# Performance work log

Hardware: AMD Instinct MI355X
Metric: run time of the kernel (lower is better)

Reference implementation:

```python
import jax, jax.numpy as jnp
import numpy as np

HIDDEN_DIM = 128
NEIGHBOR_K = 2
N_ROWS = 1_000_000
BATCH = 262_144


def setup_inputs() -> dict:
    key = jax.random.key(0)
    k1, k2, k3, k4 = jax.random.split(key, 4)
    D = HIDDEN_DIM
    cat = D * (2 * NEIGHBOR_K + 1)  # 640
    x_rows = jax.random.normal(k1, (N_ROWS, D), dtype=jnp.float32)
    seed_indices = jax.random.randint(k2, (BATCH,), 0, N_ROWS)
    # torch.nn.Linear params: W [out, in], b [out]
    W1 = jax.random.normal(k3, (D, cat), dtype=jnp.float32) * (1.0 / np.sqrt(cat))
    b1 = jnp.zeros((D,), dtype=jnp.float32)
    W2 = jax.random.normal(k4, (D, D), dtype=jnp.float32) * (1.0 / np.sqrt(D))
    b2 = jnp.zeros((D,), dtype=jnp.float32)
    return {"x_rows": x_rows, "seed_indices": seed_indices,
            "W1": W1, "b1": b1, "W2": W2, "b2": b2}


def reference(x_rows, seed_indices, W1, b1, W2, b2):
    N, D = x_rows.shape
    B = seed_indices.shape[0]
    offsets = jnp.arange(-NEIGHBOR_K, NEIGHBOR_K + 1)  # [2k+1]
    idx = jnp.clip(seed_indices[:, None] + offsets[None, :], 0, N - 1)  # [B, 2k+1]
    # gather neighbor rows and flatten -> same as torch.cat(chunks, dim=-1)
    x_cat = x_rows[idx].reshape(B, (2 * NEIGHBOR_K + 1) * D)  # [B, 5D]
    h = jax.nn.relu(x_cat @ W1.T + b1)  # [B, D]
    return h @ W2.T + b2  # [B, D]
```

## Files before the change

### kernel.cpp

```cpp
#include <hip/hip_runtime.h>
#include <hip/hip_bf16.h>

#define D 128
#define CAT 640
#define BM 32
#define W1F_ELEMS 81920
#define W2F_ELEMS 16384

typedef __attribute__((ext_vector_type(8))) short bf16x8;
typedef __attribute__((ext_vector_type(4))) float f32x4;

static __device__ __forceinline__ unsigned short f32_to_bf16(float f) {
    unsigned u = __float_as_uint(f);
    unsigned r = u + 0x7FFFu + ((u >> 16) & 1u);
    return (unsigned short)(r >> 16);
}

static __device__ __forceinline__ unsigned pack_bf16x2(float a, float b) {
    __hip_bfloat162 h = __float22bfloat162_rn(make_float2(a, b));
    return *reinterpret_cast<unsigned*>(&h);
}

static __device__ __forceinline__ void gload_lds16(const float* g, void* lds) {
    __builtin_amdgcn_global_load_lds(
        (const __attribute__((address_space(1))) void*)g,
        (__attribute__((address_space(3))) void*)lds, 16, 0, 0);
}

__global__ void prep_frags(const float* __restrict__ W1, const float* __restrict__ W2,
                           unsigned short* __restrict__ W1f, unsigned short* __restrict__ W2f) {
    int f = blockIdx.x * 256 + threadIdx.x;
    if (f < W1F_ELEMS) {
        int e = f & 7, l = (f >> 3) & 63, j16 = (f >> 9) & 7, ks = f >> 12;
        int o = j16 * 16 + (l & 15);
        int k = ks * 32 + ((l >> 4) << 3) + e;
        W1f[f] = f32_to_bf16(W1[o * CAT + k]);
    } else if (f < W1F_ELEMS + W2F_ELEMS) {
        int f2 = f - W1F_ELEMS;
        int e = f2 & 7, l = (f2 >> 3) & 63, j16 = (f2 >> 9) & 7, ks = f2 >> 12;
        int o = j16 * 16 + (l & 15);
        int k = ks * 32 + ((l >> 4) << 3) + e;
        W2f[f2] = f32_to_bf16(W2[o * D + k]);
    }
}

__global__ __launch_bounds__(256, 4) void rowmlp_kernel(
    const float* __restrict__ x_rows, const int* __restrict__ seeds,
    const unsigned short* __restrict__ W1f, const float* __restrict__ b1,
    const unsigned short* __restrict__ W2f, const float* __restrict__ b2,
    float* __restrict__ out, int Nrows)
{
    __shared__ __align__(16) unsigned char Ab[2][16384];
    __shared__ __align__(16) unsigned short Hb[16][D];
    __shared__ int sseed[BM];

    const int tid = threadIdx.x;
    const int blk = blockIdx.x;
    const int w   = tid >> 6;
    const int l   = tid & 63;
    const int l15 = l & 15;
    const int lhi = l >> 4;

    if (tid < BM) sseed[tid] = seeds[blk * BM + tid];
    __syncthreads();

    const int sb  = sseed[((w >> 1) << 4) + l15];
    const int ksb = (w & 1) * 2;

    const bf16x8* W1v = (const bf16x8*)W1f;
    const bf16x8* W2v = (const bf16x8*)W2f;

#define WAIT0 asm volatile("s_waitcnt vmcnt(0)" ::: "memory")
#define BAR   __builtin_amdgcn_s_barrier()

#define ISSUE(J, BUF)                                                          \
    {                                                                          \
        int idx = sb + (J) - 2;                                                \
        idx = idx < 0 ? 0 : (idx >= Nrows ? Nrows - 1 : idx);                  \
        const float* rp = x_rows + (size_t)idx * D + lhi * 8;                  \
        unsigned char* dst = Ab[BUF] + w * 4096;                               \
        gload_lds16(rp + (ksb + 0) * 32 + 0, dst + 0 * 1024);                  \
        gload_lds16(rp + (ksb + 0) * 32 + 4, dst + 1 * 1024);                  \
        gload_lds16(rp + (ksb + 1) * 32 + 0, dst + 2 * 1024);                  \
        gload_lds16(rp + (ksb + 1) * 32 + 4, dst + 3 * 1024);                  \
    }

#define LOADW1(J, RB)                                                          \
    {                                                                          \
        _Pragma("unroll")                                                      \
        for (int ks = 0; ks < 4; ++ks)                                         \
            _Pragma("unroll")                                                  \
            for (int n = 0; n < 2; ++n)                                        \
                w1r[RB][ks][n] = W1v[(((J) * 4 + ks) * 8 + (w * 2 + n)) * 64 + l]; \
    }

#define COMPUTE(BUF, RB)                                                       \
    {                                                                          \
        const float* fb = (const float*)Ab[BUF];                               \
        _Pragma("unroll")                                                      \
        for (int ks = 0; ks < 4; ++ks) {                                       \
            bf16x8 a[2];                                                       \
            _Pragma("unroll")                                                  \
            for (int m = 0; m < 2; ++m) {                                      \
                float4 q0 = *(const float4*)(fb + (m * 8 + ks * 2 + 0) * 256 + l * 4); \
                float4 q1 = *(const float4*)(fb + (m * 8 + ks * 2 + 1) * 256 + l * 4); \
                union { unsigned u[4]; bf16x8 v; } pk;                         \
                pk.u[0] = pack_bf16x2(q0.x, q0.y);                             \
                pk.u[1] = pack_bf16x2(q0.z, q0.w);                             \
                pk.u[2] = pack_bf16x2(q1.x, q1.y);                             \
                pk.u[3] = pack_bf16x2(q1.z, q1.w);                             \
                a[m] = pk.v;                                                   \
            }                                                                  \
            _Pragma("unroll")                                                  \
            for (int n = 0; n < 2; ++n)                                        \
                _Pragma("unroll")                                              \
                for (int m = 0; m < 2; ++m)                                    \
                    acc[m][n] = __builtin_amdgcn_mfma_f32_16x16x32_bf16(       \
                        a[m], w1r[RB][ks][n], acc[m][n], 0, 0, 0);             \
        }                                                                      \
    }

    bf16x8 w1r[2][4][2];
    f32x4 acc[2][2] = {};

    LOADW1(0, 0)
    ISSUE(0, 0)

    WAIT0; BAR;
    LOADW1(1, 1) ISSUE(1, 1)
    COMPUTE(0, 0)
    WAIT0; BAR;
    LOADW1(2, 0) ISSUE(2, 0)
    COMPUTE(1, 1)
    WAIT0; BAR;
    LOADW1(3, 1) ISSUE(3, 1)
    COMPUTE(0, 0)
    WAIT0; BAR;
    LOADW1(4, 0) ISSUE(4, 0)
    COMPUTE(1, 1)
    WAIT0; BAR;
    COMPUTE(0, 0)

    bf16x8 w2r[4][2];
    #pragma unroll
    for (int ks = 0; ks < 4; ++ks)
        #pragma unroll
        for (int n = 0; n < 2; ++n)
            w2r[ks][n] = W2v[(ks * 8 + (w * 2 + n)) * 64 + l];

    const size_t obase = (size_t)blk * BM;
    #pragma unroll
    for (int ph = 0; ph < 2; ++ph) {
        #pragma unroll
        for (int n = 0; n < 2; ++n) {
            const int col = w * 32 + n * 16 + l15;
            const float bias = b1[col];
            #pragma unroll
            for (int r = 0; r < 4; ++r) {
                const int row = lhi * 4 + r;
                float v = acc[ph][n][r] + bias;
                v = v > 0.f ? v : 0.f;
                Hb[row][col ^ (row << 3)] = f32_to_bf16(v);
            }
        }
        __syncthreads();
        f32x4 acc2[2] = {};
        #pragma unroll
        for (int ks = 0; ks < 4; ++ks) {
            bf16x8 a2 = *(const bf16x8*)(&Hb[l15][(ks * 32 + lhi * 8) ^ (l15 << 3)]);
            #pragma unroll
            for (int n = 0; n < 2; ++n)
                acc2[n] = __builtin_amdgcn_mfma_f32_16x16x32_bf16(a2, w2r[ks][n], acc2[n], 0, 0, 0);
        }
        #pragma unroll
        for (int n = 0; n < 2; ++n) {
            const int col = w * 32 + n * 16 + l15;
            const float bias = b2[col];
            #pragma unroll
            for (int r = 0; r < 4; ++r)
                out[(obase + ph * 16 + lhi * 4 + r) * D + col] = acc2[n][r] + bias;
        }
        if (ph == 0) __syncthreads();
    }
#undef ISSUE
#undef LOADW1
#undef COMPUTE
#undef WAIT0
#undef BAR
}

extern "C" void kernel_launch(void* const* d_in, const int* in_sizes, int n_in,
                              void* d_out, int out_size, void* d_ws, size_t ws_size,
                              hipStream_t stream) {
    const float* x_rows = (const float*)d_in[0];
    const int*   seeds  = (const int*)d_in[1];
    const float* W1     = (const float*)d_in[2];
    const float* b1     = (const float*)d_in[3];
    const float* W2     = (const float*)d_in[4];
    const float* b2     = (const float*)d_in[5];
    float* out = (float*)d_out;

    int Nrows = in_sizes[0] / D;
    int B = in_sizes[1];

    unsigned short* W1f = (unsigned short*)d_ws;
    unsigned short* W2f = W1f + W1F_ELEMS;

    prep_frags<<<(W1F_ELEMS + W2F_ELEMS + 255) / 256, 256, 0, stream>>>(W1, W2, W1f, W2f);
    rowmlp_kernel<<<B / BM, 256, 0, stream>>>(x_rows, seeds, W1f, b1, W2f, b2, out, Nrows);
}
```

Before: 208.5 us.

## Load W1 fragments inline, reuse gather buffer for hidden tile, single-phase second GEMM

```diff
diff --git a/kernel.cpp b/kernel.cpp
--- a/kernel.cpp
+++ b/kernel.cpp
@@ -51,7 +51,6 @@
     float* __restrict__ out, int Nrows)
 {
     __shared__ __align__(16) unsigned char Ab[2][16384];
-    __shared__ __align__(16) unsigned short Hb[16][D];
     __shared__ int sseed[BM];
 
     const int tid = threadIdx.x;
@@ -85,16 +84,7 @@
         gload_lds16(rp + (ksb + 1) * 32 + 4, dst + 3 * 1024);                  \
     }
 
-#define LOADW1(J, RB)                                                          \
-    {                                                                          \
-        _Pragma("unroll")                                                      \
-        for (int ks = 0; ks < 4; ++ks)                                         \
-            _Pragma("unroll")                                                  \
-            for (int n = 0; n < 2; ++n)                                        \
-                w1r[RB][ks][n] = W1v[(((J) * 4 + ks) * 8 + (w * 2 + n)) * 64 + l]; \
-    }
-
-#define COMPUTE(BUF, RB)                                                       \
+#define COMPUTE(BUF, J)                                                        \
     {                                                                          \
         const float* fb = (const float*)Ab[BUF];                               \
         _Pragma("unroll")                                                      \
@@ -112,78 +102,88 @@
                 a[m] = pk.v;                                                   \
             }                                                                  \
             _Pragma("unroll")                                                  \
-            for (int n = 0; n < 2; ++n)                                        \
+            for (int n = 0; n < 2; ++n) {                                      \
+                bf16x8 b = W1v[(((J) * 4 + ks) * 8 + (w * 2 + n)) * 64 + l];   \
                 _Pragma("unroll")                                              \
                 for (int m = 0; m < 2; ++m)                                    \
                     acc[m][n] = __builtin_amdgcn_mfma_f32_16x16x32_bf16(       \
-                        a[m], w1r[RB][ks][n], acc[m][n], 0, 0, 0);             \
+                        a[m], b, acc[m][n], 0, 0, 0);                          \
+            }                                                                  \
         }                                                                      \
     }
 
-    bf16x8 w1r[2][4][2];
     f32x4 acc[2][2] = {};
 
-    LOADW1(0, 0)
     ISSUE(0, 0)
 
     WAIT0; BAR;
-    LOADW1(1, 1) ISSUE(1, 1)
+    ISSUE(1, 1)
     COMPUTE(0, 0)
     WAIT0; BAR;
-    LOADW1(2, 0) ISSUE(2, 0)
+    ISSUE(2, 0)
     COMPUTE(1, 1)
     WAIT0; BAR;
-    LOADW1(3, 1) ISSUE(3, 1)
-    COMPUTE(0, 0)
-    WAIT0; BAR;
-    LOADW1(4, 0) ISSUE(4, 0)
-    COMPUTE(1, 1)
-    WAIT0; BAR;
-    COMPUTE(0, 0)
-
-    bf16x8 w2r[4][2];
+    ISSUE(3, 1)
+    COMPUTE(0, 2)
+    WAIT0; BAR;
+    ISSUE(4, 0)
+    COMPUTE(1, 3)
+    WAIT0; BAR;
+    COMPUTE(0, 4)
+
+    unsigned short (*Hb)[D] = (unsigned short (*)[D])Ab[1];
     #pragma unroll
-    for (int ks = 0; ks < 4; ++ks)
-        #pragma unroll
-        for (int n = 0; n < 2; ++n)
-            w2r[ks][n] = W2v[(ks * 8 + (w * 2 + n)) * 64 + l];
-
-    const size_t obase = (size_t)blk * BM;
-    #pragma unroll
-    for (int ph = 0; ph < 2; ++ph) {
-        #pragma unroll
-        for (int n = 0; n < 2; ++n) {
-            const int col = w * 32 + n * 16 + l15;
-            const float bias = b1[col];
+    for (int n = 0; n < 2; ++n) {
+        const int col = w * 32 + n * 16 + l15;
+        const float bias = b1[col];
+        #pragma unroll
+        for (int m = 0; m < 2; ++m) {
             #pragma unroll
             for (int r = 0; r < 4; ++r) {
-                const int row = lhi * 4 + r;
-                float v = acc[ph][n][r] + bias;
+                float v = acc[m][n][r] + bias;
                 v = v > 0.f ? v : 0.f;
-                Hb[row][col ^ (row << 3)] = f32_to_bf16(v);
+                const int row = m * 16 + lhi * 4 + r;
+                Hb[row][col ^ ((row & 7) << 3)] = f32_to_bf16(v);
             }
         }
-        __syncthreads();
-        f32x4 acc2[2] = {};
-        #pragma unroll
-        for (int ks = 0; ks < 4; ++ks) {
-            bf16x8 a2 = *(const bf16x8*)(&Hb[l15][(ks * 32 + lhi * 8) ^ (l15 << 3)]);
+    }
+    __syncthreads();
+
+    f32x4 acc2[2][2] = {};
+    #pragma unroll
+    for (int ks = 0; ks < 4; ++ks) {
+        bf16x8 a2[2], bb[2];
+        #pragma unroll
+        for (int m = 0; m < 2; ++m) {
+            const int row = m * 16 + l15;
+            a2[m] = *(const bf16x8*)(&Hb[row][(ks * 32 + lhi * 8) ^ ((row & 7) << 3)]);
+        }
+        #pragma unroll
+        for (int n = 0; n < 2; ++n) {
+            const int j16 = w * 2 + n;
+            bb[n] = W2v[(ks * 8 + j16) * 64 + l];
+        }
+        #pragma unroll
+        for (int m = 0; m < 2; ++m)
             #pragma unroll
             for (int n = 0; n < 2; ++n)
-                acc2[n] = __builtin_amdgcn_mfma_f32_16x16x32_bf16(a2, w2r[ks][n], acc2[n], 0, 0, 0);
-        }
-        #pragma unroll
-        for (int n = 0; n < 2; ++n) {
-            const int col = w * 32 + n * 16 + l15;
-            const float bias = b2[col];
+                acc2[m][n] = __builtin_amdgcn_mfma_f32_16x16x32_bf16(a2[m], bb[n], acc2[m][n], 0, 0, 0);
+    }
+
+    #pragma unroll
+    for (int n = 0; n < 2; ++n) {
+        const int col = w * 32 + n * 16 + l15;
+        const float bias = b2[col];
+        #pragma unroll
+        for (int m = 0; m < 2; ++m) {
             #pragma unroll
-            for (int r = 0; r < 4; ++r)
-                out[(obase + ph * 16 + lhi * 4 + r) * D + col] = acc2[n][r] + bias;
-        }
-        if (ph == 0) __syncthreads();
+            for (int r = 0; r < 4; ++r) {
+                const int row = m * 16 + lhi * 4 + r;
+                out[(size_t)(blk * BM + row) * D + col] = acc2[m][n][r] + bias;
+            }
+        }
     }
 #undef ISSUE
-#undef LOADW1
 #undef COMPUTE
 #undef WAIT0
 #undef BAR
```

New measurement: 215.4 us. +3.3%, slower.
